# Optimization experiments

Measured on AMD Instinct MI355X. Metric: run time of the kernel, lower is better.

The kernel has to match this reference:

```python
import jax, jax.numpy as jnp
import numpy as np
import math

D_MODEL = 1024
D_STATE = 64
D_CONV = 4
EXPAND = 2
D_INNER = EXPAND * D_MODEL
DT_RANK = max(16, D_MODEL // 16)
SEQ_LEN = 2048
BATCH = 4

def setup_inputs() -> dict:
    key = jax.random.key(0)
    ks = jax.random.split(key, 16)
    s = lambda *sh: 1.0 / math.sqrt(sh[-1])
    x = jax.random.normal(ks[0], (SEQ_LEN, BATCH, D_MODEL), jnp.float32)
    state = jnp.zeros((BATCH, D_INNER, D_STATE), jnp.float32)
    W_in = jax.random.normal(ks[1], (2 * D_INNER, D_MODEL), jnp.float32) * s(2 * D_INNER, D_MODEL)
    b_in = jnp.zeros((2 * D_INNER,), jnp.float32)
    conv_w = jax.random.normal(ks[2], (D_INNER, 1, D_CONV), jnp.float32) * s(1, D_CONV)
    conv_b = jnp.zeros((D_INNER,), jnp.float32)
    W_xp = jax.random.normal(ks[3], (DT_RANK + 2 * D_STATE, D_INNER), jnp.float32) * s(1, D_INNER)
    b_xp = jnp.zeros((DT_RANK + 2 * D_STATE,), jnp.float32)
    W_dt = jax.random.normal(ks[4], (D_INNER, DT_RANK), jnp.float32) * s(1, DT_RANK)
    # dt bias init as in module: softplus-inverse of dt in [1e-3, 0.1]
    dt = jnp.exp(jax.random.uniform(ks[5], (D_INNER,)) * (math.log(0.1) - math.log(0.001)) + math.log(0.001))
    b_dt = dt + jnp.log(-jnp.expm1(-dt))
    A_log = jnp.log(jnp.broadcast_to(jnp.arange(1, D_STATE + 1, dtype=jnp.float32)[None, :], (D_INNER, D_STATE)))
    D = jnp.ones((D_INNER,), jnp.float32)
    W_out = jax.random.normal(ks[6], (D_MODEL, D_INNER), jnp.float32) * s(1, D_INNER)
    b_out = jnp.zeros((D_MODEL,), jnp.float32)
    ln_g = jnp.ones((D_MODEL,), jnp.float32)
    ln_b = jnp.zeros((D_MODEL,), jnp.float32)
    return dict(x=x, state=state, W_in=W_in, b_in=b_in, conv_w=conv_w, conv_b=conv_b,
                W_xp=W_xp, b_xp=b_xp, W_dt=W_dt, b_dt=b_dt, A_log=A_log, D=D,
                W_out=W_out, b_out=b_out, ln_g=ln_g, ln_b=ln_b)

def _silu(v):
    return v * jax.nn.sigmoid(v)

def _forward(x, state, W_in, b_in, conv_w, conv_b, W_xp, b_xp, W_dt, b_dt, A_log, D, W_out, b_out, ln_g, ln_b):
    S, B, _ = x.shape
    xz = x @ W_in.T + b_in                      # [S,B,2*di]
    x_inner, z = jnp.split(xz, 2, axis=-1)      # [S,B,di] each
    # causal depthwise conv1d: pad left (d_conv-1), matching conv1d(pad=K-1)[..., :S]
    xc = jnp.transpose(x_inner, (1, 2, 0))      # [B,di,S]
    xc = jax.lax.conv_general_dilated(
        xc, conv_w, window_strides=(1,), padding=[(D_CONV - 1, 0)],
        dimension_numbers=('NCH', 'OIH', 'NCH'), feature_group_count=D_INNER)
    xc = xc + conv_b[None, :, None]
    x_conv = _silu(jnp.transpose(xc, (2, 0, 1)))  # [S,B,di]
    # input-dependent projections over full sequence
    xp = x_conv @ W_xp.T + b_xp                 # [S,B,dt_rank+2*ds]
    dt_low, B_seq, C_seq = jnp.split(xp, [DT_RANK, DT_RANK + D_STATE], axis=-1)
    # NOTE: original adds dt_proj.bias twice (Linear already includes it)
    dt = jax.nn.softplus(dt_low @ W_dt.T + 2.0 * b_dt)  # [S,B,di]
    A = -jnp.exp(A_log)                         # [di,ds]

    def step(carry, inp):
        dt_t, B_t, C_t, x_t = inp               # [B,di],[B,ds],[B,ds],[B,di]
        dA = jnp.exp(dt_t[..., None] * A)       # [B,di,ds]
        dBx = (dt_t * x_t)[..., None] * B_t[:, None, :]  # [B,di,ds]
        new = carry * dA + dBx
        y = jnp.einsum('bdn,bn->bd', new, C_t) + D * x_t
        return new, y

    final_state, ys = jax.lax.scan(step, state, (dt, B_seq, C_seq, x_conv))
    ys = ys * _silu(z)                          # [S,B,di]
    out = jnp.mean(ys, axis=0) @ W_out.T + b_out  # [B,d_model]
    mu = jnp.mean(out, axis=-1, keepdims=True)
    var = jnp.var(out, axis=-1, keepdims=True)
    out = (out - mu) / jnp.sqrt(var + 1e-5) * ln_g + ln_b
    return out, final_state

def reference(x, state, W_in, b_in, conv_w, conv_b, W_xp, b_xp, W_dt, b_dt, A_log, D, W_out, b_out, ln_g, ln_b):
    return _forward(x, state, W_in, b_in, conv_w, conv_b, W_xp, b_xp, W_dt, b_dt, A_log, D, W_out, b_out, ln_g, ln_b)
```

## Files before the change

### kernel.cpp

```cpp
#include <hip/hip_runtime.h>
#include <hip/hip_fp16.h>

typedef __attribute__((ext_vector_type(8))) short short8;
typedef __attribute__((ext_vector_type(8))) unsigned short u16x8;
typedef __attribute__((ext_vector_type(4))) float f32x4;

#define S_LEN 2048
#define BATCH 4
#define DM 1024
#define DI 2048
#define DS 64
#define DTR 64
#define XPW 192
#define NCH 8
#define CLEN 256

typedef const __attribute__((address_space(4))) unsigned* cu_as4;

__device__ __forceinline__ unsigned short f2bf(float f){
  unsigned u = __builtin_bit_cast(unsigned, f);
  u += 0x7fffu + ((u >> 16) & 1u);
  return (unsigned short)(u >> 16);
}
__device__ __forceinline__ float bf2f(unsigned short h){
  unsigned u = ((unsigned)h) << 16;
  return __builtin_bit_cast(float, u);
}
__device__ __forceinline__ void gload16(const void* g, void* l){
  __builtin_amdgcn_global_load_lds((const __attribute__((address_space(1))) void*)g,
                                   (__attribute__((address_space(3))) void*)l, 16, 0, 0);
}
__device__ __forceinline__ float siluf_(float v){ return v / (1.f + __expf(-v)); }

__global__ __launch_bounds__(256) void cvt_all_k(const float* __restrict__ i0, unsigned short* __restrict__ o0,
                                                 const float* __restrict__ i1, unsigned short* __restrict__ o1,
                                                 const float* __restrict__ i2, unsigned short* __restrict__ o2,
                                                 const float* __restrict__ i3, unsigned short* __restrict__ o3)
{
  int bid = blockIdx.x;
  const float* in; unsigned short* out; int base;
  if (bid < 8192)       { in = i0; out = o0; base = bid; }
  else if (bid < 12288) { in = i1; out = o1; base = bid - 8192; }
  else if (bid < 12672) { in = i2; out = o2; base = bid - 12288; }
  else                  { in = i3; out = o3; base = bid - 12672; }
  int i = (base * 256 + threadIdx.x) * 4;
  float4 v = *(const float4*)(in + i);
  ushort4 o;
  o.x = f2bf(v.x); o.y = f2bf(v.y); o.z = f2bf(v.z); o.w = f2bf(v.w);
  *(ushort4*)(out + i) = o;
}

template<int EPI>
__global__ __launch_bounds__(256)
void gemm_bt(const unsigned short* __restrict__ A, const unsigned short* __restrict__ B,
             const float* __restrict__ bias,
             int N, int K, int lda, int ldb,
             void* __restrict__ vp0, void* __restrict__ vp1,
             const void* __restrict__ vp2, const void* __restrict__ vp3, int nsilu)
{
  __shared__ unsigned short As[128 * 32];
  __shared__ unsigned short Bs[128 * 32];
  const int tid  = threadIdx.x;
  const int lane = tid & 63;
  const int wid  = tid >> 6;
  int bm, bn;
  if constexpr (EPI == 2) {
    int flat = blockIdx.y * 64 + blockIdx.x;
    int swz = (flat & 7) * 256 + (flat >> 3);
    bm = swz & 63; bn = swz >> 6;
  } else {
    bm = blockIdx.x; bn = blockIdx.y;
  }
  int k_lo = 0, k_hi = K;
  if constexpr (EPI == 3) { k_lo = blockIdx.z * 512; k_hi = k_lo + 512; }
  const int r0 = tid >> 2;
  const int c0 = (tid & 3) * 8;
  int brow0 = bn * 128 + r0;        if (brow0 > N - 1) brow0 = N - 1;
  int brow1 = bn * 128 + 64 + r0;   if (brow1 > N - 1) brow1 = N - 1;
  const unsigned short* pa0 = A + (size_t)(bm * 128 + r0) * lda + c0;
  const unsigned short* pa1 = A + (size_t)(bm * 128 + 64 + r0) * lda + c0;
  const unsigned short* pb0 = B + (size_t)brow0 * ldb + c0;
  const unsigned short* pb1 = B + (size_t)brow1 * ldb + c0;
  f32x4 acc[4][4] = {};
  const int fr = lane & 15, fq = lane >> 4;
  const int wm = (wid >> 1) * 64, wn = (wid & 1) * 64;
  const int aoff0 = (wm + fr) * 32 + fq * 8;
  const int boff0 = (wn + fr) * 32 + fq * 8;
  for (int k0 = k_lo; k0 < k_hi; k0 += 32) {
    __syncthreads();
    gload16(pa0 + k0, &As[tid * 8]);
    gload16(pa1 + k0, &As[2048 + tid * 8]);
    gload16(pb0 + k0, &Bs[tid * 8]);
    gload16(pb1 + k0, &Bs[2048 + tid * 8]);
    __syncthreads();
    short8 av[4], bv[4];
#pragma unroll
    for (int i = 0; i < 4; i++) av[i] = *(const short8*)&As[aoff0 + i * 16 * 32];
#pragma unroll
    for (int i = 0; i < 4; i++) bv[i] = *(const short8*)&Bs[boff0 + i * 16 * 32];
#pragma unroll
    for (int i = 0; i < 4; i++)
#pragma unroll
      for (int j = 0; j < 4; j++)
        acc[i][j] = __builtin_amdgcn_mfma_f32_16x16x32_bf16(av[i], bv[j], acc[i][j], 0, 0, 0);
  }

  if constexpr (EPI == 3) {
    float* xpp = (float*)vp0;
    const size_t kb = (size_t)blockIdx.z * 8192 * 256;
#pragma unroll
    for (int i = 0; i < 4; i++) {
#pragma unroll
      for (int j = 0; j < 4; j++) {
        int gc = bn * 128 + wn + j * 16 + fr;
#pragma unroll
        for (int e = 0; e < 4; e++) {
          int gr = bm * 128 + wm + i * 16 + fq * 4 + e;
          xpp[kb + (size_t)gr * 256 + gc] = acc[i][j][e];
        }
      }
    }
  } else if constexpr (EPI == 2) {
    unsigned short* xib = (unsigned short*)vp0;
    unsigned short* grm = (unsigned short*)vp1;
#pragma unroll
    for (int i = 0; i < 4; i++) {
#pragma unroll
      for (int j = 0; j < 4; j++) {
        int gc = bn * 128 + wn + j * 16 + fr;
        float bb = bias[gc];
#pragma unroll
        for (int e = 0; e < 4; e++) {
          int gr = bm * 128 + wm + i * 16 + fq * 4 + e;
          float v = acc[i][j][e] + bb;
          if (gc < nsilu) xib[(size_t)gr * DI + gc] = f2bf(v);
          else            grm[(size_t)gr * DI + (gc - nsilu)] = f2bf(siluf_(v));
        }
      }
    }
  } else {
    unsigned* dtH = (unsigned*)vp0;
    unsigned* dxg = (unsigned*)vp1;
    const unsigned short* xcb = (const unsigned short*)vp2;
    const unsigned short* grm = (const unsigned short*)vp3;
#pragma unroll
    for (int j = 0; j < 4; j++) {
      int gc = bn * 128 + wn + j * 16 + fr;
      float bb2 = 2.f * bias[gc];
#pragma unroll
      for (int i = 0; i < 4; i++)
#pragma unroll
        for (int e = 0; e < 4; e++) {
          float v = acc[i][j][e] + bb2;
          acc[i][j][e] = fmaxf(v, 0.f) + log1pf(__expf(-fabsf(v)));
        }
    }
    __shared__ unsigned short hbuf[256 * 36];
    const int myc = wn >> 6;
    const int tbase = wm / 4;
    for (int cc = 0; cc < 2; ++cc) {
      __syncthreads();
      if (myc == cc) {
#pragma unroll
        for (int i = 0; i < 4; i++)
#pragma unroll
          for (int j = 0; j < 4; j++) {
            int dl = j * 16 + fr;
            int t_ = tbase + i * 4 + fq;
#pragma unroll
            for (int e = 0; e < 4; e++)
              hbuf[(e * 64 + dl) * 36 + t_] =
                __builtin_bit_cast(unsigned short, __float2half_rn(acc[i][j][e]));
          }
      }
      __syncthreads();
#pragma unroll
      for (int k = 0; k < 4; ++k) {
        int gidx = tid + k * 256;
        int t   = gidx & 31;
        int gl8 = (gidx >> 5) & 7;
        int e   = gidx >> 8;
        int R   = e * 64 + gl8 * 8;
        uint4 o;
        o.x = (unsigned)hbuf[(R+0)*36 + t] | ((unsigned)hbuf[(R+1)*36 + t] << 16);
        o.y = (unsigned)hbuf[(R+2)*36 + t] | ((unsigned)hbuf[(R+3)*36 + t] << 16);
        o.z = (unsigned)hbuf[(R+4)*36 + t] | ((unsigned)hbuf[(R+5)*36 + t] << 16);
        o.w = (unsigned)hbuf[(R+6)*36 + t] | ((unsigned)hbuf[(R+7)*36 + t] << 16);
        size_t G = (size_t)(bn * 16 + cc * 8 + gl8);
        *(uint4*)&dtH[(((size_t)e * 256 + G) * 2048 + bm * 32 + t) * 4] = o;
      }
#pragma unroll
      for (int k = 0; k < 4; ++k) {
        int gidx = tid + k * 256;
        int t   = gidx & 31;
        int gl8 = (gidx >> 5) & 7;
        int e   = gidx >> 8;
        int gr  = (bm * 32 + t) * 4 + e;
        int col = bn * 128 + cc * 64 + gl8 * 8;
        u16x8 xv = *(const u16x8*)&xcb[(size_t)gr * DI + col];
        u16x8 gv = *(const u16x8*)&grm[(size_t)gr * DI + col];
        int R = e * 64 + gl8 * 8;
        unsigned ow[8];
#pragma unroll
        for (int u = 0; u < 8; ++u) {
          float dt = __half2float(__builtin_bit_cast(__half, hbuf[(R + u) * 36 + t]));
          float dtx = dt * bf2f((unsigned short)xv[u]);
          ow[u] = ((unsigned)f2bf(dtx) << 16) | (unsigned)(unsigned short)gv[u];
        }
        size_t G = (size_t)(bn * 16 + cc * 8 + gl8);
        unsigned* dst = &dxg[(((size_t)e * 256 + G) * 2048 + bm * 32 + t) * 8];
        uint4 o0, o1;
        o0.x = ow[0]; o0.y = ow[1]; o0.z = ow[2]; o0.w = ow[3];
        o1.x = ow[4]; o1.y = ow[5]; o1.z = ow[6]; o1.w = ow[7];
        *(uint4*)dst = o0;
        *(uint4*)(dst + 4) = o1;
      }
    }
  }
}

__global__ __launch_bounds__(192) void xpred_k(const float* __restrict__ xpp,
                                               const float* __restrict__ bias,
                                               unsigned short* __restrict__ xpb,
                                               float* __restrict__ bcI)
{
  const int gr = blockIdx.x;
  const int gc = threadIdx.x;
  const size_t o = (size_t)gr * 256 + gc;
  float v = xpp[o] + xpp[o + 2097152] + xpp[o + 2 * 2097152] + xpp[o + 3 * 2097152] + bias[gc];
  xpb[(size_t)gr * XPW + gc] = f2bf(v);
  if (gc >= 64 && gc < 128)      bcI[((size_t)gr * 64 + gc - 64) * 2 + 0] = v;
  else if (gc >= 128)            bcI[((size_t)gr * 64 + gc - 128) * 2 + 1] = v;
}

__global__ __launch_bounds__(256) void convsxg_k(const unsigned short* __restrict__ xib,
                                                 const unsigned short* __restrict__ grm,
                                                 const float* __restrict__ cw,
                                                 const float* __restrict__ cb,
                                                 unsigned short* __restrict__ xcb,
                                                 float* __restrict__ sxg)
{
  const int d4 = blockIdx.x * 1024 + threadIdx.x * 4;
  const int b  = blockIdx.y;
  const int t0 = blockIdx.z * 16;
  float4 cwv[4]; float cbv[4];
#pragma unroll
  for (int j = 0; j < 4; ++j) { cwv[j] = *(const float4*)&cw[(d4 + j) * 4]; cbv[j] = cb[d4 + j]; }
  ushort4 z4; z4.x = z4.y = z4.z = z4.w = 0;
  ushort4 xm1 = (t0 >= 1) ? *(const ushort4*)&xib[((size_t)((t0 - 1) * 4 + b)) * DI + d4] : z4;
  ushort4 xm2 = (t0 >= 2) ? *(const ushort4*)&xib[((size_t)((t0 - 2) * 4 + b)) * DI + d4] : z4;
  ushort4 xm3 = (t0 >= 3) ? *(const ushort4*)&xib[((size_t)((t0 - 3) * 4 + b)) * DI + d4] : z4;
  float sa[4] = {0.f, 0.f, 0.f, 0.f};
  for (int tt = 0; tt < 16; ++tt) {
    const int t = t0 + tt;
    const size_t row = ((size_t)(t * 4 + b)) * DI + d4;
    ushort4 x0 = *(const ushort4*)&xib[row];
    ushort4 gv = *(const ushort4*)&grm[row];
    unsigned short xr[4] = {x0.x, x0.y, x0.z, x0.w};
    unsigned short r1[4] = {xm1.x, xm1.y, xm1.z, xm1.w};
    unsigned short r2[4] = {xm2.x, xm2.y, xm2.z, xm2.w};
    unsigned short r3[4] = {xm3.x, xm3.y, xm3.z, xm3.w};
    unsigned short gg[4] = {gv.x, gv.y, gv.z, gv.w};
    unsigned short ov[4];
#pragma unroll
    for (int j = 0; j < 4; ++j) {
      float s = cbv[j];
      s = fmaf(cwv[j].w, bf2f(xr[j]), s);
      s = fmaf(cwv[j].z, bf2f(r1[j]), s);
      s = fmaf(cwv[j].y, bf2f(r2[j]), s);
      s = fmaf(cwv[j].x, bf2f(r3[j]), s);
      ov[j] = f2bf(siluf_(s));
      sa[j] = fmaf(bf2f(ov[j]), bf2f(gg[j]), sa[j]);
    }
    ushort4 o; o.x = ov[0]; o.y = ov[1]; o.z = ov[2]; o.w = ov[3];
    *(ushort4*)&xcb[row] = o;
    xm3 = xm2; xm2 = xm1; xm1 = x0;
  }
#pragma unroll
  for (int j = 0; j < 4; ++j) atomicAdd(&sxg[b * DI + d4 + j], sa[j]);
}

__global__ __launch_bounds__(256) void scan_k(const unsigned* __restrict__ dtHg,
                                              const unsigned* __restrict__ dxgg,
                                              const float* __restrict__ bcI,
                                              const float* __restrict__ A_log,
                                              float* __restrict__ Pb,
                                              float* __restrict__ Eb,
                                              float* __restrict__ Fb,
                                              float* __restrict__ accp)
{
  const int tid  = threadIdx.x;
  const int lane = tid & 63;
  const int gw = __builtin_amdgcn_readfirstlane(blockIdx.x * 4 + (tid >> 6));
  const int b  = gw >> 11;
  const int c  = (gw >> 8) & 7;
  const int g  = gw & 255;
  const int d0 = g * 8;
  const float LOG2E = 1.4426950408889634f;
  float a2[8], st[8], Dr[8], Fr[8], acc[8];
#pragma unroll
  for (int j = 0; j < 8; ++j) {
    a2[j] = -__expf(A_log[(size_t)(d0 + j) * DS + lane]) * LOG2E;
    st[j] = 0.f; Dr[j] = 1.f; Fr[j] = 0.f; acc[j] = 0.f;
  }
  cu_as4 pdt = (cu_as4)(unsigned long long)(dtHg + (((size_t)(b * 256 + g)) * S_LEN + c * CLEN) * 4);
  cu_as4 pdx = (cu_as4)(unsigned long long)(dxgg + (((size_t)(b * 256 + g)) * S_LEN + c * CLEN) * 8);
  const float* pbc = bcI + (((size_t)(c * CLEN) * 4 + b) * 64 + lane) * 2;
#pragma unroll 2
  for (int t = 0; t < CLEN; ++t) {
    unsigned dw0 = pdt[t * 4 + 0], dw1 = pdt[t * 4 + 1];
    unsigned dw2 = pdt[t * 4 + 2], dw3 = pdt[t * 4 + 3];
    unsigned xs[8];
#pragma unroll
    for (int j = 0; j < 8; ++j) xs[j] = pdx[t * 8 + j];
    float2 bc = *(const float2*)(pbc + (size_t)t * 512);
    float dts[8];
    dts[0] = __half2float(__builtin_bit_cast(__half, (unsigned short)(dw0 & 0xffffu)));
    dts[1] = __half2float(__builtin_bit_cast(__half, (unsigned short)(dw0 >> 16)));
    dts[2] = __half2float(__builtin_bit_cast(__half, (unsigned short)(dw1 & 0xffffu)));
    dts[3] = __half2float(__builtin_bit_cast(__half, (unsigned short)(dw1 >> 16)));
    dts[4] = __half2float(__builtin_bit_cast(__half, (unsigned short)(dw2 & 0xffffu)));
    dts[5] = __half2float(__builtin_bit_cast(__half, (unsigned short)(dw2 >> 16)));
    dts[6] = __half2float(__builtin_bit_cast(__half, (unsigned short)(dw3 & 0xffffu)));
    dts[7] = __half2float(__builtin_bit_cast(__half, (unsigned short)(dw3 >> 16)));
#pragma unroll
    for (int j = 0; j < 8; ++j) {
      float dxs = __builtin_bit_cast(float, xs[j] & 0xffff0000u);
      float gsv = __builtin_bit_cast(float, xs[j] << 16);
      float dA = __builtin_amdgcn_exp2f(dts[j] * a2[j]);
      st[j] = fmaf(st[j], dA, dxs * bc.x);
      Dr[j] *= dA;
      float w = gsv * bc.y;
      acc[j] = fmaf(st[j], w, acc[j]);
      Fr[j] = fmaf(Dr[j], w, Fr[j]);
    }
  }
  const size_t sb = (((size_t)((b * NCH + c) * 256 + g)) * 8) * 64 + lane;
#pragma unroll
  for (int j = 0; j < 8; ++j) {
    Pb[sb + j * 64] = st[j];
    Eb[sb + j * 64] = Dr[j];
    Fb[sb + j * 64] = Fr[j];
  }
#pragma unroll
  for (int j = 0; j < 8; ++j)
#pragma unroll
    for (int m = 32; m; m >>= 1) acc[j] += __shfl_xor(acc[j], m, 64);
  if (lane == 0) {
#pragma unroll
    for (int j = 0; j < 8; ++j)
      accp[(b * NCH + c) * DI + d0 + j] = acc[j];
  }
}

__global__ __launch_bounds__(256) void fixup_k(const float* __restrict__ Pb,
                                               const float* __restrict__ Eb,
                                               const float* __restrict__ Fb,
                                               const float* __restrict__ accp,
                                               const float* __restrict__ state_in,
                                               float* __restrict__ accbuf,
                                               float* __restrict__ state_out)
{
  const int tid  = threadIdx.x;
  const int lane = tid & 63;
  const int gw = blockIdx.x * 4 + (tid >> 6);
  const int b  = gw >> 8;
  const int g  = gw & 255;
  const int d0 = g * 8;
  float S[8], v[8];
#pragma unroll
  for (int j = 0; j < 8; ++j) {
    S[j] = state_in[((size_t)(b * DI + d0 + j)) * DS + lane];
    v[j] = 0.f;
  }
#pragma unroll
  for (int c = 0; c < NCH; ++c) {
    const size_t sb = (((size_t)((b * NCH + c) * 256 + g)) * 8) * 64 + lane;
#pragma unroll
    for (int j = 0; j < 8; ++j) {
      float P = Pb[sb + j * 64], E = Eb[sb + j * 64], F = Fb[sb + j * 64];
      v[j] = fmaf(F, S[j], v[j]);
      S[j] = fmaf(E, S[j], P);
    }
  }
#pragma unroll
  for (int j = 0; j < 8; ++j)
    state_out[((size_t)(b * DI + d0 + j)) * DS + lane] = S[j];
#pragma unroll
  for (int j = 0; j < 8; ++j)
#pragma unroll
    for (int m = 32; m; m >>= 1) v[j] += __shfl_xor(v[j], m, 64);
  if (lane == 0) {
#pragma unroll
    for (int j = 0; j < 8; ++j) {
      float s = v[j];
#pragma unroll
      for (int c = 0; c < NCH; ++c) s += accp[(b * NCH + c) * DI + d0 + j];
      accbuf[b * DI + d0 + j] = s;
    }
  }
}

__global__ __launch_bounds__(256) void out_gemm_k(const float* __restrict__ accb,
                                                  const float* __restrict__ sxg,
                                                  const float* __restrict__ Dv,
                                                  const float* __restrict__ W_out,
                                                  const float* __restrict__ b_out,
                                                  float* __restrict__ outpre)
{
  int b = blockIdx.y;
  int m = blockIdx.x * 8 + (threadIdx.x >> 5);
  int dl = threadIdx.x & 31;
  const float* wr = W_out + (size_t)m * DI;
  const float* ac = accb + b * DI;
  const float* sx = sxg + b * DI;
  float p = 0.f;
  for (int dd = dl; dd < DI; dd += 32) {
    float av = fmaf(Dv[dd], sx[dd], ac[dd]);
    p = fmaf(wr[dd], av, p);
  }
#pragma unroll
  for (int s = 16; s; s >>= 1) p += __shfl_xor(p, s, 32);
  if (dl == 0) outpre[b * DM + m] = p * (1.f / 2048.f) + b_out[m];
}

__global__ __launch_bounds__(256) void ln_k(const float* __restrict__ outpre,
                                            const float* __restrict__ g,
                                            const float* __restrict__ bta,
                                            float* __restrict__ dout)
{
  int b = blockIdx.x;
  const float* row = outpre + b * DM;
  float s = 0.f, s2 = 0.f, vv[4];
#pragma unroll
  for (int i = 0; i < 4; i++) {
    float v = row[threadIdx.x + i * 256];
    vv[i] = v; s += v; s2 += v * v;
  }
#pragma unroll
  for (int m = 32; m; m >>= 1) { s += __shfl_xor(s, m, 64); s2 += __shfl_xor(s2, m, 64); }
  __shared__ float rs[4], rs2[4];
  int w = threadIdx.x >> 6;
  if ((threadIdx.x & 63) == 0) { rs[w] = s; rs2[w] = s2; }
  __syncthreads();
  float S = rs[0] + rs[1] + rs[2] + rs[3];
  float S2 = rs2[0] + rs2[1] + rs2[2] + rs2[3];
  float mu = S * (1.f / 1024.f);
  float var = S2 * (1.f / 1024.f) - mu * mu;
  float inv = rsqrtf(var + 1e-5f);
#pragma unroll
  for (int i = 0; i < 4; i++) {
    int c = threadIdx.x + i * 256;
    dout[b * DM + c] = (vv[i] - mu) * inv * g[c] + bta[c];
  }
}

extern "C" void kernel_launch(void* const* d_in, const int* in_sizes, int n_in,
                              void* d_out, int out_size, void* d_ws, size_t ws_size,
                              hipStream_t stream)
{
  const float* x      = (const float*)d_in[0];
  const float* state0 = (const float*)d_in[1];
  const float* W_in   = (const float*)d_in[2];
  const float* b_in   = (const float*)d_in[3];
  const float* conv_w = (const float*)d_in[4];
  const float* conv_b = (const float*)d_in[5];
  const float* W_xp   = (const float*)d_in[6];
  const float* b_xp   = (const float*)d_in[7];
  const float* W_dt   = (const float*)d_in[8];
  const float* b_dt   = (const float*)d_in[9];
  const float* A_log  = (const float*)d_in[10];
  const float* Dvec   = (const float*)d_in[11];
  const float* W_out  = (const float*)d_in[12];
  const float* b_out  = (const float*)d_in[13];
  const float* ln_g   = (const float*)d_in[14];
  const float* ln_b   = (const float*)d_in[15];
  float* out = (float*)d_out;

  const size_t MB = 1024 * 1024;
  char* ws = (char*)d_ws;
  unsigned short* grm  = (unsigned short*)(ws + 0);
  unsigned short* xcb  = (unsigned short*)(ws + 32  * MB);
  unsigned short* xib  = (unsigned short*)(ws + 64  * MB);
  unsigned*       dtH  = (unsigned*)(ws + 64  * MB);
  unsigned short* xb   = (unsigned short*)(ws + 96  * MB);
  unsigned short* wbin = (unsigned short*)(ws + 112 * MB);
  float*          xpp  = (float*)(ws + 96 * MB);
  unsigned*       dxg  = (unsigned*)(ws + 96  * MB);
  unsigned short* xpb  = (unsigned short*)(ws + 160 * MB);
  float*          bcI  = (float*)(ws + 163 * MB);
  unsigned short* wbxp = (unsigned short*)(ws + 167 * MB);
  unsigned short* wbdt = (unsigned short*)(ws + 167 * MB + 786432);
  float*          sxg    = (float*)(ws + 168 * MB);
  float*          accb   = (float*)(ws + 168 * MB + 32768);
  float*          outpre = (float*)(ws + 168 * MB + 65536);
  float*          Pb   = (float*)(ws + 0);
  float*          Eb   = (float*)(ws + 16 * MB);
  float*          Fb   = (float*)(ws + 32 * MB);
  float*          accp = (float*)(ws + 48 * MB);

  cvt_all_k<<<12800, 256, 0, stream>>>(x, xb, W_in, wbin, W_xp, wbxp, W_dt, wbdt);
  hipMemsetAsync(sxg, 0, 4 * DI * sizeof(float), stream);
  gemm_bt<2><<<dim3(64, 32), 256, 0, stream>>>(xb, wbin, b_in, 4096, 1024, 1024, 1024,
                                               xib, grm, nullptr, nullptr, 2048);
  convsxg_k<<<dim3(2, 4, 128), 256, 0, stream>>>(xib, grm, conv_w, conv_b, xcb, sxg);
  gemm_bt<3><<<dim3(64, 2, 4), 256, 0, stream>>>(xcb, wbxp, nullptr, 192, 2048, 2048, 2048,
                                                 xpp, nullptr, nullptr, nullptr, 0);
  xpred_k<<<8192, 192, 0, stream>>>(xpp, b_xp, xpb, bcI);
  gemm_bt<1><<<dim3(64, 16), 256, 0, stream>>>(xpb, wbdt, b_dt, 2048, 64, XPW, 64,
                                               dtH, dxg, xcb, grm, 0);
  scan_k<<<2048, 256, 0, stream>>>(dtH, dxg, bcI, A_log, Pb, Eb, Fb, accp);
  fixup_k<<<256, 256, 0, stream>>>(Pb, Eb, Fb, accp, state0, accb, out + 4096);
  out_gemm_k<<<dim3(128, 4), 256, 0, stream>>>(accb, sxg, Dvec, W_out, b_out, outpre);
  ln_k<<<4, 256, 0, stream>>>(outpre, ln_g, ln_b, out);
}
```

Before: 505.5 us.

## Double scan chunk count and recompute chunk decay from per-chunk dt sums

Splits the sequence scan into 16 chunks of 128 steps instead of 8 of 256, doubling the number of parallel scan waves. Instead of writing the per-chunk cumulative decay (Eb) from the scan, the dt-projection GEMM epilogue atomically accumulates per-chunk dt sums. The fixup kernel then recomputes the decay as exp2(a*sum dt). This removes one large buffer write and read but adds atomics in the GEMM epilogue and twice the fixup chunk iterations. The fp16-rounded dt sums may also shift numerics slightly.

```diff
diff --git a/kernel.cpp b/kernel.cpp
--- a/kernel.cpp
+++ b/kernel.cpp
@@ -12,8 +12,8 @@
 #define DS 64
 #define DTR 64
 #define XPW 192
-#define NCH 8
-#define CLEN 256
+#define NCH 16
+#define CLEN 128
 
 typedef const __attribute__((address_space(4))) unsigned* cu_as4;
 
@@ -56,7 +56,8 @@
              const float* __restrict__ bias,
              int N, int K, int lda, int ldb,
              void* __restrict__ vp0, void* __restrict__ vp1,
-             const void* __restrict__ vp2, const void* __restrict__ vp3, int nsilu)
+             const void* __restrict__ vp2, const void* __restrict__ vp3,
+             int nsilu, float* __restrict__ sdt)
 {
   __shared__ unsigned short As[128 * 32];
   __shared__ unsigned short Bs[128 * 32];
@@ -158,6 +159,7 @@
     __shared__ unsigned short hbuf[256 * 36];
     const int myc = wn >> 6;
     const int tbase = wm / 4;
+    const int chk = bm >> 2;
     for (int cc = 0; cc < 2; ++cc) {
       __syncthreads();
       if (myc == cc) {
@@ -214,6 +216,16 @@
         o1.x = ow[4]; o1.y = ow[5]; o1.z = ow[6]; o1.w = ow[7];
         *(uint4*)dst = o0;
         *(uint4*)(dst + 4) = o1;
+      }
+      {
+        int e  = tid >> 6;
+        int dl = tid & 63;
+        float s = 0.f;
+#pragma unroll
+        for (int t = 0; t < 32; ++t)
+          s += __half2float(__builtin_bit_cast(__half, hbuf[(e * 64 + dl) * 36 + t]));
+        int g8 = bn * 16 + cc * 8 + (dl >> 3);
+        atomicAdd(&sdt[(((size_t)e * NCH + chk) * 256 + g8) * 8 + (dl & 7)], s);
       }
     }
   }
@@ -285,15 +297,14 @@
                                               const float* __restrict__ bcI,
                                               const float* __restrict__ A_log,
                                               float* __restrict__ Pb,
-                                              float* __restrict__ Eb,
                                               float* __restrict__ Fb,
                                               float* __restrict__ accp)
 {
   const int tid  = threadIdx.x;
   const int lane = tid & 63;
   const int gw = __builtin_amdgcn_readfirstlane(blockIdx.x * 4 + (tid >> 6));
-  const int b  = gw >> 11;
-  const int c  = (gw >> 8) & 7;
+  const int b  = gw >> 12;
+  const int c  = (gw >> 8) & 15;
   const int g  = gw & 255;
   const int d0 = g * 8;
   const float LOG2E = 1.4426950408889634f;
@@ -339,7 +350,6 @@
 #pragma unroll
   for (int j = 0; j < 8; ++j) {
     Pb[sb + j * 64] = st[j];
-    Eb[sb + j * 64] = Dr[j];
     Fb[sb + j * 64] = Fr[j];
   }
 #pragma unroll
@@ -354,9 +364,10 @@
 }
 
 __global__ __launch_bounds__(256) void fixup_k(const float* __restrict__ Pb,
-                                               const float* __restrict__ Eb,
                                                const float* __restrict__ Fb,
+                                               const float* __restrict__ sdt,
                                                const float* __restrict__ accp,
+                                               const float* __restrict__ A_log,
                                                const float* __restrict__ state_in,
                                                float* __restrict__ accbuf,
                                                float* __restrict__ state_out)
@@ -367,18 +378,22 @@
   const int b  = gw >> 8;
   const int g  = gw & 255;
   const int d0 = g * 8;
-  float S[8], v[8];
+  const float LOG2E = 1.4426950408889634f;
+  float a2[8], S[8], v[8];
 #pragma unroll
   for (int j = 0; j < 8; ++j) {
+    a2[j] = -__expf(A_log[(size_t)(d0 + j) * DS + lane]) * LOG2E;
     S[j] = state_in[((size_t)(b * DI + d0 + j)) * DS + lane];
     v[j] = 0.f;
   }
 #pragma unroll
   for (int c = 0; c < NCH; ++c) {
     const size_t sb = (((size_t)((b * NCH + c) * 256 + g)) * 8) * 64 + lane;
+    const size_t se = (((size_t)(b * NCH + c)) * 256 + g) * 8;
 #pragma unroll
     for (int j = 0; j < 8; ++j) {
-      float P = Pb[sb + j * 64], E = Eb[sb + j * 64], F = Fb[sb + j * 64];
+      float P = Pb[sb + j * 64], F = Fb[sb + j * 64];
+      float E = __builtin_amdgcn_exp2f(a2[j] * sdt[se + j]);
       v[j] = fmaf(F, S[j], v[j]);
       S[j] = fmaf(E, S[j], P);
     }
@@ -492,25 +507,25 @@
   unsigned short* wbxp = (unsigned short*)(ws + 167 * MB);
   unsigned short* wbdt = (unsigned short*)(ws + 167 * MB + 786432);
   float*          sxg    = (float*)(ws + 168 * MB);
-  float*          accb   = (float*)(ws + 168 * MB + 32768);
-  float*          outpre = (float*)(ws + 168 * MB + 65536);
+  float*          sdt    = (float*)(ws + 168 * MB + 32768);
+  float*          accb   = (float*)(ws + 168 * MB + 557056);
+  float*          outpre = (float*)(ws + 168 * MB + 589824);
+  float*          accp   = (float*)(ws + 168 * MB + 606208);
   float*          Pb   = (float*)(ws + 0);
-  float*          Eb   = (float*)(ws + 16 * MB);
   float*          Fb   = (float*)(ws + 32 * MB);
-  float*          accp = (float*)(ws + 48 * MB);
 
   cvt_all_k<<<12800, 256, 0, stream>>>(x, xb, W_in, wbin, W_xp, wbxp, W_dt, wbdt);
-  hipMemsetAsync(sxg, 0, 4 * DI * sizeof(float), stream);
+  hipMemsetAsync(sxg, 0, 557056, stream);
   gemm_bt<2><<<dim3(64, 32), 256, 0, stream>>>(xb, wbin, b_in, 4096, 1024, 1024, 1024,
-                                               xib, grm, nullptr, nullptr, 2048);
+                                               xib, grm, nullptr, nullptr, 2048, nullptr);
   convsxg_k<<<dim3(2, 4, 128), 256, 0, stream>>>(xib, grm, conv_w, conv_b, xcb, sxg);
   gemm_bt<3><<<dim3(64, 2, 4), 256, 0, stream>>>(xcb, wbxp, nullptr, 192, 2048, 2048, 2048,
-                                                 xpp, nullptr, nullptr, nullptr, 0);
+                                                 xpp, nullptr, nullptr, nullptr, 0, nullptr);
   xpred_k<<<8192, 192, 0, stream>>>(xpp, b_xp, xpb, bcI);
   gemm_bt<1><<<dim3(64, 16), 256, 0, stream>>>(xpb, wbdt, b_dt, 2048, 64, XPW, 64,
-                                               dtH, dxg, xcb, grm, 0);
-  scan_k<<<2048, 256, 0, stream>>>(dtH, dxg, bcI, A_log, Pb, Eb, Fb, accp);
-  fixup_k<<<256, 256, 0, stream>>>(Pb, Eb, Fb, accp, state0, accb, out + 4096);
+                                               dtH, dxg, xcb, grm, 0, sdt);
+  scan_k<<<4096, 256, 0, stream>>>(dtH, dxg, bcI, A_log, Pb, Fb, accp);
+  fixup_k<<<256, 256, 0, stream>>>(Pb, Fb, sdt, accp, A_log, state0, accb, out + 4096);
   out_gemm_k<<<dim3(128, 4), 256, 0, stream>>>(accb, sxg, Dvec, W_out, b_out, outpre);
   ln_k<<<4, 256, 0, stream>>>(outpre, ln_g, ln_b, out);
 }
```

Result: no change. 501.4 us (-0.8%).
